# Kernel tuning notes

Measured on AMD Instinct MI355X. Metric: run time of the kernel, lower is better.

The kernel has to match this reference:

```python
import jax, jax.numpy as jnp
import numpy as np

N_NODES = 50000
N_EDGES = 600000
FEAT = 128
N_LAYERS = 4


def setup_inputs() -> dict:
    key = jax.random.key(0)
    ks = jax.random.split(key, 7)
    feats = jax.random.normal(ks[0], (N_NODES, FEAT), dtype=jnp.float32)
    src = jax.random.randint(ks[1], (N_EDGES,), 0, N_NODES)
    dst = jax.random.randint(ks[2], (N_EDGES,), 0, N_NODES)
    s = 1.0 / np.sqrt(FEAT)  # torch Linear default init range
    theta_w = jax.random.uniform(ks[3], (N_LAYERS, FEAT, FEAT), jnp.float32, -s, s)
    theta_b = jax.random.uniform(ks[4], (N_LAYERS, FEAT), jnp.float32, -s, s)
    phi_w = jax.random.uniform(ks[5], (N_LAYERS, FEAT, FEAT), jnp.float32, -s, s)
    phi_b = jax.random.uniform(ks[6], (N_LAYERS, FEAT), jnp.float32, -s, s)
    return {"feats": feats, "src": src, "dst": dst,
            "theta_w": theta_w, "theta_b": theta_b,
            "phi_w": phi_w, "phi_b": phi_b}


def _edgeconv(x, src, dst, tw, tb, pw, pb):
    # EdgeConv (Wang et al. 2018): out_i = max_{(j->i) in E} theta(x_j - x_i) + phi(x_i)
    phi = x @ pw.T + pb                       # [N, F] node-level linear (avoid per-edge recompute)
    diff = x[src] - x[dst]                    # [E, F] gather
    msg = diff @ tw.T + tb + phi[dst]         # [E, F]
    agg = jax.ops.segment_max(msg, dst, num_segments=x.shape[0])  # [N, F]
    # nodes with no incoming edges get -inf from segment_max; zero them (DGL convention)
    return jnp.where(jnp.isneginf(agg), jnp.zeros_like(agg), agg)


def reference(feats, src, dst, theta_w, theta_b, phi_w, phi_b):
    x = feats
    for l in range(N_LAYERS):
        x = _edgeconv(x, src, dst, theta_w[l], theta_b[l], phi_w[l], phi_b[l])
        x = jax.nn.relu(x)
    return x
```

## Files before the change

### kernel.cpp

```cpp
#include <hip/hip_runtime.h>

#define FEAT 128
#define SLABS 4

typedef __attribute__((ext_vector_type(8))) _Float16 f16x8;
typedef __attribute__((ext_vector_type(2))) _Float16 f16x2;
typedef __attribute__((ext_vector_type(4))) float f32x4;

static __device__ __forceinline__ int wave_incl_scan(int v, int lane) {
#pragma unroll
    for (int off = 1; off < 64; off <<= 1) {
        int u = __shfl_up(v, off, 64);
        if (lane >= off) v += u;
    }
    return v;
}


__global__ void prep_kernel(const int* __restrict__ src, const int* __restrict__ dst,
                            int* __restrict__ deg4, int E, int slab_size,
                            const float* __restrict__ tw, const float* __restrict__ pw,
                            const float* __restrict__ tb, const float* __restrict__ pb,
                            _Float16* __restrict__ wt, _Float16* __restrict__ wp,
                            float* __restrict__ bsum, int wn, int nbias,
                            const float* __restrict__ x, _Float16* __restrict__ x16, int xn4,
                            int hb, int wb) {
    int bid = blockIdx.x;
    if (bid < hb) {
        int e = bid * 256 + threadIdx.x;
        if (e < E) {
            int sl = src[e] / slab_size;
            atomicAdd(&deg4[dst[e] * SLABS + sl], 1);
        }
    } else if (bid < hb + wb) {
        int i = (bid - hb) * 256 + threadIdx.x;
        if (i < wn) { wt[i] = (_Float16)tw[i]; wp[i] = (_Float16)pw[i]; }
        if (i < nbias) bsum[i] = tb[i] + pb[i];
    } else {
        int i = (bid - hb - wb) * 256 + threadIdx.x;
        if (i < xn4) {
            float4 v = ((const float4*)x)[i];
            f16x2 a, b;
            a[0] = (_Float16)v.x; a[1] = (_Float16)v.y;
            b[0] = (_Float16)v.z; b[1] = (_Float16)v.w;
            ((f16x2*)x16)[i * 2] = a;
            ((f16x2*)x16)[i * 2 + 1] = b;
        }
    }
}


__global__ __launch_bounds__(1024) void scan1_kernel(const int* __restrict__ deg,
                                                     int* __restrict__ row_ptr,
                                                     int* __restrict__ bsum, int N4) {
    int i = blockIdx.x * 1024 + threadIdx.x;
    int lane = threadIdx.x & 63;
    int w = threadIdx.x >> 6;
    int v = (i < N4) ? deg[i] : 0;
    int inc = wave_incl_scan(v, lane);
    __shared__ int wsum[16];
    if (lane == 63) wsum[w] = inc;
    __syncthreads();
    if (w == 0) {
        int s = (lane < 16) ? wsum[lane] : 0;
        int si = wave_incl_scan(s, lane);
        if (lane < 16) wsum[lane] = si - s;
    }
    __syncthreads();
    int exc = inc - v + wsum[w];
    if (i < N4) row_ptr[i] = exc;
    if (threadIdx.x == 1023) bsum[blockIdx.x] = exc + v;
}

__global__ __launch_bounds__(1024) void scan2_kernel(const int* __restrict__ bsum,
                                                     int* __restrict__ boff,
                                                     int* __restrict__ row_ptr,
                                                     int nb, int N4, int E) {
    int tid = threadIdx.x;
    int lane = tid & 63;
    int w = tid >> 6;
    int v = (tid < nb) ? bsum[tid] : 0;
    int inc = wave_incl_scan(v, lane);
    __shared__ int wsum[16];
    if (lane == 63) wsum[w] = inc;
    __syncthreads();
    if (w == 0) {
        int s = (lane < 16) ? wsum[lane] : 0;
        int si = wave_incl_scan(s, lane);
        if (lane < 16) wsum[lane] = si - s;
    }
    __syncthreads();
    if (tid < nb) boff[tid] = inc - v + wsum[w];
    if (tid == 0) row_ptr[N4] = E;
}

__global__ void scan3_kernel(int* __restrict__ row_ptr, const int* __restrict__ boff, int N4) {
    int i = blockIdx.x * blockDim.x + threadIdx.x;
    if (i < N4) row_ptr[i] += boff[i >> 10];
}


static __device__ __forceinline__ void gemm_body(
        int bx,
        const _Float16* __restrict__ x16,
        const _Float16* __restrict__ wt, const _Float16* __restrict__ wp,
        const float* __restrict__ bias,
        _Float16* __restrict__ t16, _Float16* __restrict__ q16, int M) {
    int lane = threadIdx.x & 63;
    int l16 = lane & 15;
    int quad = lane >> 4;
    int cn0 = (threadIdx.x >> 6) * 32;

    f16x8 bt[2][4], bp[2][4];
    float biasv[2];
#pragma unroll
    for (int ct = 0; ct < 2; ++ct) {
        int col = cn0 + ct * 16 + l16;
        biasv[ct] = bias[col];
#pragma unroll
        for (int kk = 0; kk < 4; ++kk) {
            int k = kk * 32 + quad * 8;
            bt[ct][kk] = *(const f16x8*)(wt + (size_t)col * FEAT + k);
            bp[ct][kk] = *(const f16x8*)(wp + (size_t)col * FEAT + k);
        }
    }

    int rbase0 = bx * 128;
#pragma unroll 1
    for (int rs = 0; rs < 8; ++rs) {
        int rbase = rbase0 + rs * 16;
        int row = rbase + l16;
        int rowc = (row < M) ? row : (M - 1);
        f16x8 a[4];
#pragma unroll
        for (int kk = 0; kk < 4; ++kk)
            a[kk] = *(const f16x8*)(x16 + (size_t)rowc * FEAT + kk * 32 + quad * 8);

        f32x4 accT[2] = {{0.f, 0.f, 0.f, 0.f}, {0.f, 0.f, 0.f, 0.f}};
        f32x4 accP[2] = {{0.f, 0.f, 0.f, 0.f}, {0.f, 0.f, 0.f, 0.f}};
#pragma unroll
        for (int kk = 0; kk < 4; ++kk) {
#pragma unroll
            for (int ct = 0; ct < 2; ++ct) {
                accT[ct] = __builtin_amdgcn_mfma_f32_16x16x32_f16(a[kk], bt[ct][kk], accT[ct], 0, 0, 0);
                accP[ct] = __builtin_amdgcn_mfma_f32_16x16x32_f16(a[kk], bp[ct][kk], accP[ct], 0, 0, 0);
            }
        }
#pragma unroll
        for (int ct = 0; ct < 2; ++ct) {
            int col = cn0 + ct * 16 + l16;
#pragma unroll
            for (int r = 0; r < 4; ++r) {
                int ro = rbase + quad * 4 + r;
                if (ro < M) {
                    t16[(size_t)ro * FEAT + col] = (_Float16)accT[ct][r];
                    q16[(size_t)ro * FEAT + col] =
                        (_Float16)(accP[ct][r] - accT[ct][r] + biasv[ct]);
                }
            }
        }
    }
}

__global__ __launch_bounds__(256) void mfma_gemm_kernel(
        const _Float16* __restrict__ x16,
        const _Float16* __restrict__ wt, const _Float16* __restrict__ wp,
        const float* __restrict__ bias,
        _Float16* __restrict__ t16, _Float16* __restrict__ q16, int M) {
    gemm_body(blockIdx.x, x16, wt, wp, bias, t16, q16, M);
}

__global__ __launch_bounds__(256) void fused0_kernel(
        const _Float16* __restrict__ x16,
        const _Float16* __restrict__ wt, const _Float16* __restrict__ wp,
        const float* __restrict__ bias,
        _Float16* __restrict__ t16, _Float16* __restrict__ q16, int M, int gb,
        const int* __restrict__ src, const int* __restrict__ dst,
        const int* __restrict__ row_ptr4, int* __restrict__ fill4,
        int* __restrict__ esrc, int E, int slab_size) {
    if ((int)blockIdx.x < gb) {
        gemm_body(blockIdx.x, x16, wt, wp, bias, t16, q16, M);
    } else {
        int e = (blockIdx.x - gb) * 256 + threadIdx.x;
        if (e < E) {
            int s = src[e];
            int key = dst[e] * SLABS + s / slab_size;
            int pos = row_ptr4[key] + atomicAdd(&fill4[key], 1);
            esrc[pos] = s;
        }
    }
}


static __device__ __forceinline__ f16x8 vmax8(f16x8 a, f16x8 b) {
#pragma unroll
    for (int i = 0; i < 8; ++i) a[i] = (a[i] > b[i]) ? a[i] : b[i];
    return a;
}

__global__ __launch_bounds__(256) void agg_kernel(
        const _Float16* __restrict__ t16, const _Float16* __restrict__ q16,
        const int* __restrict__ row_ptr4, const int* __restrict__ esrc,
        float* __restrict__ outf, _Float16* __restrict__ ox, int N, int E) {
    int wv = threadIdx.x >> 6;
    int lane = threadIdx.x & 63;
    int node0 = (blockIdx.x * 4 + wv) * 4;
    if (node0 >= N) return;

    int g = lane >> 4;
    int c = lane & 15;
    int nodeg = node0 + g;
    bool nvalid = nodeg < N;

    int rpmax = SLABS * N;
    int rpidx = SLABS * node0 + (lane < 17 ? lane : 16);
    if (rpidx > rpmax) rpidx = rpmax;
    int rp = row_ptr4[rpidx];

    const _Float16 NEGINF = (_Float16)(-65504.0f);
    f16x8 m0, m1, m2, m3;
#pragma unroll
    for (int i = 0; i < 8; ++i) { m0[i] = NEGINF; m1[i] = NEGINF; m2[i] = NEGINF; m3[i] = NEGINF; }

#pragma unroll 1
    for (int s = 0; s < SLABS; ++s) {
        int beg = __shfl(rp, SLABS * g + s);
        int end = __shfl(rp, SLABS * g + s + 1);
        int cnt = end - beg;
        int cm = cnt;
        cm = max(cm, __shfl_xor(cm, 16, 64));
        cm = max(cm, __shfl_xor(cm, 32, 64));

        for (int base = 0; base < cm; base += 16) {
            int rem = cnt - base;
            int off = (c < rem) ? c : (rem > 0 ? rem - 1 : 0);
            int a = beg + base + off;
            if (a < 0) a = 0;
            if (a >= E) a = E - 1;
            int myidx = esrc[a];
            int kend = cm - base; if (kend > 16) kend = 16;
            int k = 0;
            for (; k + 4 <= kend; k += 4) {
                int i0 = __shfl(myidx, 16 * g + k);
                int i1 = __shfl(myidx, 16 * g + k + 1);
                int i2 = __shfl(myidx, 16 * g + k + 2);
                int i3 = __shfl(myidx, 16 * g + k + 3);
                bool p0 = (k < rem), p1 = (k + 1 < rem), p2 = (k + 2 < rem), p3 = (k + 3 < rem);
                f16x8 v0, v1, v2, v3;
                if (p0) v0 = *(const f16x8*)(t16 + (size_t)i0 * FEAT + c * 8);
                if (p1) v1 = *(const f16x8*)(t16 + (size_t)i1 * FEAT + c * 8);
                if (p2) v2 = *(const f16x8*)(t16 + (size_t)i2 * FEAT + c * 8);
                if (p3) v3 = *(const f16x8*)(t16 + (size_t)i3 * FEAT + c * 8);
                if (p0) m0 = vmax8(m0, v0);
                if (p1) m1 = vmax8(m1, v1);
                if (p2) m2 = vmax8(m2, v2);
                if (p3) m3 = vmax8(m3, v3);
            }
            for (; k < kend; ++k) {
                int idx = __shfl(myidx, 16 * g + k);
                if (k < rem) {
                    f16x8 v = *(const f16x8*)(t16 + (size_t)idx * FEAT + c * 8);
                    m0 = vmax8(m0, v);
                }
            }
        }
    }

    f16x8 m = vmax8(vmax8(m0, m1), vmax8(m2, m3));

    if (nvalid) {
        f16x8 qi = *(const f16x8*)(q16 + (size_t)nodeg * FEAT + c * 8);
        float o[8];
#pragma unroll
        for (int i = 0; i < 8; ++i)
            o[i] = fmaxf((float)m[i] + (float)qi[i], 0.f);

        if (outf) {
            float4 o0 = make_float4(o[0], o[1], o[2], o[3]);
            float4 o1 = make_float4(o[4], o[5], o[6], o[7]);
            ((float4*)(outf + (size_t)nodeg * FEAT + c * 8))[0] = o0;
            ((float4*)(outf + (size_t)nodeg * FEAT + c * 8))[1] = o1;
        }
        if (ox) {
            f16x8 oh;
#pragma unroll
            for (int i = 0; i < 8; ++i) oh[i] = (_Float16)o[i];
            *(f16x8*)(ox + (size_t)nodeg * FEAT + c * 8) = oh;
        }
    }
}


extern "C" void kernel_launch(void* const* d_in, const int* in_sizes, int n_in,
                              void* d_out, int out_size, void* d_ws, size_t ws_size,
                              hipStream_t stream) {
    const float* feats   = (const float*)d_in[0];
    const int*   src     = (const int*)d_in[1];
    const int*   dst     = (const int*)d_in[2];
    const float* theta_w = (const float*)d_in[3];
    const float* theta_b = (const float*)d_in[4];
    const float* phi_w   = (const float*)d_in[5];
    const float* phi_b   = (const float*)d_in[6];

    const int N = in_sizes[0] / FEAT;
    const int E = in_sizes[1];
    const int L = in_sizes[3] / (FEAT * FEAT);
    const int N4 = N * SLABS;
    const int slab_size = (N + SLABS - 1) / SLABS;

    char* ws = (char*)d_ws;
    size_t off = 0;
    auto alloc = [&](size_t bytes) -> void* {
        void* ptr = ws + off;
        off = (off + bytes + 255) & ~(size_t)255;
        return ptr;
    };
    _Float16* t16 = (_Float16*)alloc((size_t)N * FEAT * 2);
    _Float16* q16 = (_Float16*)alloc((size_t)N * FEAT * 2);
    _Float16* x16 = (_Float16*)alloc((size_t)N * FEAT * 2);
    _Float16* wt16 = (_Float16*)alloc((size_t)L * FEAT * FEAT * 2);
    _Float16* wp16 = (_Float16*)alloc((size_t)L * FEAT * FEAT * 2);
    float* bsum_b = (float*)alloc((size_t)L * FEAT * sizeof(float));
    int* deg4     = (int*)alloc((size_t)N4 * sizeof(int));
    int* fill4    = (int*)alloc((size_t)N4 * sizeof(int));
    int* row_ptr4 = (int*)alloc((size_t)(N4 + 1) * sizeof(int));
    int* esrc     = (int*)alloc((size_t)E * sizeof(int));
    int* bsum     = (int*)alloc(2048 * sizeof(int));
    int* boff     = (int*)alloc(2048 * sizeof(int));
    (void)ws_size;

    hipMemsetAsync(deg4, 0, (size_t)N4 * sizeof(int), stream);
    hipMemsetAsync(fill4, 0, (size_t)N4 * sizeof(int), stream);

    int eb = (E + 255) / 256;
    int wn = L * FEAT * FEAT;
    int wb = (wn + 255) / 256;
    int xn4 = N * FEAT / 4;
    int xb = (xn4 + 255) / 256;
    prep_kernel<<<eb + wb + xb, 256, 0, stream>>>(
        src, dst, deg4, E, slab_size,
        theta_w, phi_w, theta_b, phi_b, wt16, wp16, bsum_b, wn, L * FEAT,
        feats, x16, xn4, eb, wb);

    int nb = (N4 + 1023) >> 10;
    scan1_kernel<<<nb, 1024, 0, stream>>>(deg4, row_ptr4, bsum, N4);
    scan2_kernel<<<1, 1024, 0, stream>>>(bsum, boff, row_ptr4, nb, N4, E);
    scan3_kernel<<<(N4 + 255) / 256, 256, 0, stream>>>(row_ptr4, boff, N4);

    int gb = (N + 127) / 128;
    int ab = (N + 15) / 16;
    for (int l = 0; l < L; ++l) {
        if (l == 0) {
            fused0_kernel<<<gb + eb, 256, 0, stream>>>(
                x16, wt16, wp16, bsum_b, t16, q16, N, gb,
                src, dst, row_ptr4, fill4, esrc, E, slab_size);
        } else {
            mfma_gemm_kernel<<<gb, 256, 0, stream>>>(
                x16,
                wt16 + (size_t)l * FEAT * FEAT,
                wp16 + (size_t)l * FEAT * FEAT,
                bsum_b + (size_t)l * FEAT,
                t16, q16, N);
        }

        bool last = (l == L - 1);
        agg_kernel<<<ab, 256, 0, stream>>>(
            t16, q16,
            row_ptr4, esrc,
            last ? (float*)d_out : nullptr,
            last ? nullptr : x16,
            N, E);
    }
}
```

Before: 318.5 us.

## Assign one wave per node in aggregation, splitting edges across 16-lane groups

The aggregation kernel moves from four nodes per wave (one 16-lane group per node, looping over four slabs) to one node per wave. The four lane groups each take a different edge, results are merged with cross-lane xor shuffles, and each lane writes two output features. The aim is better load balance across nodes with uneven degree and more gathers in flight per node, since the slab loop and per-group trip-count divergence go away. In exchange it launches four times as many blocks, adds shuffle reductions, and issues redundant loads when a node has fewer edges than the 8-edge step (padding re-reads edge 0).

```diff
diff --git a/kernel.cpp b/kernel.cpp
--- a/kernel.cpp
+++ b/kernel.cpp
@@ -198,95 +198,74 @@
     return a;
 }
 
+static __device__ __forceinline__ f16x8 shfl_xor8(f16x8 v, int m) {
+    union { f16x8 h; int i[4]; } u, r;
+    u.h = v;
+#pragma unroll
+    for (int d = 0; d < 4; ++d) r.i[d] = __shfl_xor(u.i[d], m, 64);
+    return r.h;
+}
+
 __global__ __launch_bounds__(256) void agg_kernel(
         const _Float16* __restrict__ t16, const _Float16* __restrict__ q16,
         const int* __restrict__ row_ptr4, const int* __restrict__ esrc,
         float* __restrict__ outf, _Float16* __restrict__ ox, int N, int E) {
     int wv = threadIdx.x >> 6;
     int lane = threadIdx.x & 63;
-    int node0 = (blockIdx.x * 4 + wv) * 4;
-    if (node0 >= N) return;
+    int node = blockIdx.x * 4 + wv;
+    if (node >= N) return;
+    (void)E;
 
     int g = lane >> 4;
     int c = lane & 15;
-    int nodeg = node0 + g;
-    bool nvalid = nodeg < N;
-
-    int rpmax = SLABS * N;
-    int rpidx = SLABS * node0 + (lane < 17 ? lane : 16);
-    if (rpidx > rpmax) rpidx = rpmax;
-    int rp = row_ptr4[rpidx];
+
+    int beg = row_ptr4[node * SLABS];
+    int end = row_ptr4[node * SLABS + SLABS];
+    int cnt = end - beg;
+
+    f16x2 qv = *(const f16x2*)(q16 + (size_t)node * FEAT + c * 8 + g * 2);
 
     const _Float16 NEGINF = (_Float16)(-65504.0f);
-    f16x8 m0, m1, m2, m3;
-#pragma unroll
-    for (int i = 0; i < 8; ++i) { m0[i] = NEGINF; m1[i] = NEGINF; m2[i] = NEGINF; m3[i] = NEGINF; }
-
-#pragma unroll 1
-    for (int s = 0; s < SLABS; ++s) {
-        int beg = __shfl(rp, SLABS * g + s);
-        int end = __shfl(rp, SLABS * g + s + 1);
-        int cnt = end - beg;
-        int cm = cnt;
-        cm = max(cm, __shfl_xor(cm, 16, 64));
-        cm = max(cm, __shfl_xor(cm, 32, 64));
-
-        for (int base = 0; base < cm; base += 16) {
-            int rem = cnt - base;
-            int off = (c < rem) ? c : (rem > 0 ? rem - 1 : 0);
-            int a = beg + base + off;
-            if (a < 0) a = 0;
-            if (a >= E) a = E - 1;
-            int myidx = esrc[a];
-            int kend = cm - base; if (kend > 16) kend = 16;
-            int k = 0;
-            for (; k + 4 <= kend; k += 4) {
-                int i0 = __shfl(myidx, 16 * g + k);
-                int i1 = __shfl(myidx, 16 * g + k + 1);
-                int i2 = __shfl(myidx, 16 * g + k + 2);
-                int i3 = __shfl(myidx, 16 * g + k + 3);
-                bool p0 = (k < rem), p1 = (k + 1 < rem), p2 = (k + 2 < rem), p3 = (k + 3 < rem);
-                f16x8 v0, v1, v2, v3;
-                if (p0) v0 = *(const f16x8*)(t16 + (size_t)i0 * FEAT + c * 8);
-                if (p1) v1 = *(const f16x8*)(t16 + (size_t)i1 * FEAT + c * 8);
-                if (p2) v2 = *(const f16x8*)(t16 + (size_t)i2 * FEAT + c * 8);
-                if (p3) v3 = *(const f16x8*)(t16 + (size_t)i3 * FEAT + c * 8);
-                if (p0) m0 = vmax8(m0, v0);
-                if (p1) m1 = vmax8(m1, v1);
-                if (p2) m2 = vmax8(m2, v2);
-                if (p3) m3 = vmax8(m3, v3);
-            }
-            for (; k < kend; ++k) {
-                int idx = __shfl(myidx, 16 * g + k);
-                if (k < rem) {
-                    f16x8 v = *(const f16x8*)(t16 + (size_t)idx * FEAT + c * 8);
-                    m0 = vmax8(m0, v);
-                }
-            }
-        }
-    }
-
-    f16x8 m = vmax8(vmax8(m0, m1), vmax8(m2, m3));
-
-    if (nvalid) {
-        f16x8 qi = *(const f16x8*)(q16 + (size_t)nodeg * FEAT + c * 8);
-        float o[8];
-#pragma unroll
-        for (int i = 0; i < 8; ++i)
-            o[i] = fmaxf((float)m[i] + (float)qi[i], 0.f);
-
-        if (outf) {
-            float4 o0 = make_float4(o[0], o[1], o[2], o[3]);
-            float4 o1 = make_float4(o[4], o[5], o[6], o[7]);
-            ((float4*)(outf + (size_t)nodeg * FEAT + c * 8))[0] = o0;
-            ((float4*)(outf + (size_t)nodeg * FEAT + c * 8))[1] = o1;
-        }
-        if (ox) {
-            f16x8 oh;
-#pragma unroll
-            for (int i = 0; i < 8; ++i) oh[i] = (_Float16)o[i];
-            *(f16x8*)(ox + (size_t)nodeg * FEAT + c * 8) = oh;
-        }
+    f16x8 m0, m1;
+#pragma unroll
+    for (int i = 0; i < 8; ++i) { m0[i] = NEGINF; m1[i] = NEGINF; }
+
+    for (int cb = 0; cb < cnt; cb += 64) {
+        int lim = cnt - cb; if (lim > 64) lim = 64;
+        int a = beg + cb + (lane < lim ? lane : 0);
+        int myidx = esrc[a];
+        for (int base = 0; base < lim; base += 8) {
+            int e0 = base + g;     if (e0 >= lim) e0 = 0;
+            int e1 = base + 4 + g; if (e1 >= lim) e1 = 0;
+            int i0 = __shfl(myidx, e0, 64);
+            int i1 = __shfl(myidx, e1, 64);
+            f16x8 v0 = *(const f16x8*)(t16 + (size_t)i0 * FEAT + c * 8);
+            f16x8 v1 = *(const f16x8*)(t16 + (size_t)i1 * FEAT + c * 8);
+            m0 = vmax8(m0, v0);
+            m1 = vmax8(m1, v1);
+        }
+    }
+
+    f16x8 mm = vmax8(m0, m1);
+    mm = vmax8(mm, shfl_xor8(mm, 16));
+    mm = vmax8(mm, shfl_xor8(mm, 32));
+
+    union { f16x8 h; int i[4]; } um; um.h = mm;
+    int w01 = (g & 1) ? um.i[1] : um.i[0];
+    int w23 = (g & 1) ? um.i[3] : um.i[2];
+    int w = (g & 2) ? w23 : w01;
+    union { int i; f16x2 h; } uw; uw.i = w;
+
+    float o0 = fmaxf((float)uw.h[0] + (float)qv[0], 0.f);
+    float o1 = fmaxf((float)uw.h[1] + (float)qv[1], 0.f);
+
+    if (outf) {
+        float2 ov = make_float2(o0, o1);
+        *(float2*)(outf + (size_t)node * FEAT + c * 8 + g * 2) = ov;
+    }
+    if (ox) {
+        f16x2 oh; oh[0] = (_Float16)o0; oh[1] = (_Float16)o1;
+        *(f16x2*)(ox + (size_t)node * FEAT + c * 8 + g * 2) = oh;
     }
 }
 
@@ -348,7 +327,7 @@
     scan3_kernel<<<(N4 + 255) / 256, 256, 0, stream>>>(row_ptr4, boff, N4);
 
     int gb = (N + 127) / 128;
-    int ab = (N + 15) / 16;
+    int ab = (N + 3) / 4;
     for (int l = 0; l < L; ++l) {
         if (l == 0) {
             fused0_kernel<<<gb + eb, 256, 0, stream>>>(
```

Result: no change. 317.9 us (-0.2%).
